# Kernel optimization log

Measured on AMD Instinct MI355X. Metric: run time of the kernel, lower is better.

## Reference

```python
import jax, jax.numpy as jnp
import numpy as np

# ---- graph / model config (matches init_kwargs) ----
N_FUNC, N_IN, N_OUT = 10000, 2000, 2000
C = 8          # hidden channels per function node (fix_hidden_channels=True)
K_FF = 16      # function->function in-degree
K_IF = 4       # out-edges per input node
LAYERS = 4     # shared ResBlock applied `layers` times
B = 64
EPS = 1e-5
N_NODES = N_FUNC + N_IN + N_OUT
H = N_FUNC * C


def _build_graph():
    """Homogeneous edge list ordered [f->f, in->f, f->out] like hetero2homo,
    plus COO indices of W1 (E x H) and W3 (H x E) per get_conv_indices."""
    rng = np.random.default_rng(0)
    ff_dst = np.repeat(np.arange(N_FUNC), K_FF)
    ff_src = rng.integers(0, N_FUNC, ff_dst.shape[0])
    if_src = np.repeat(np.arange(N_IN) + N_FUNC, K_IF)
    if_dst = rng.integers(0, N_FUNC, if_src.shape[0])
    fo_dst = np.arange(N_OUT) + N_FUNC + N_IN
    fo_src = rng.integers(0, N_FUNC, N_OUT)
    src = np.concatenate([ff_src, if_src, fo_src]).astype(np.int32)
    dst = np.concatenate([ff_dst, if_dst, fo_dst]).astype(np.int32)
    # W1: edge e (dst = function node j) -> hidden channels j*C + c
    e1 = np.nonzero(dst < N_FUNC)[0]
    w1_row = np.repeat(e1, C).astype(np.int32)
    w1_col = (np.repeat(dst[e1].astype(np.int64), C) * C + np.tile(np.arange(C), e1.shape[0])).astype(np.int32)
    # W3: hidden channel src*C + c -> edge e (src = function node)
    e3 = np.nonzero(src < N_FUNC)[0]
    w3_col = np.repeat(e3, C).astype(np.int32)
    w3_row = (np.repeat(src[e3].astype(np.int64), C) * C + np.tile(np.arange(C), e3.shape[0])).astype(np.int32)
    return src, dst, w1_row, w1_col, w3_row, w3_col


def setup_inputs() -> dict:
    src, dst, w1_row, w1_col, w3_row, w3_col = _build_graph()
    key = jax.random.key(0)
    k0, k1, k2 = jax.random.split(key, 3)
    s1 = 1.0 / np.sqrt(K_FF * C)   # fan-based scale for W1 values
    s3 = 1.0 / np.sqrt(C)          # fan-based scale for W3 values
    E = src.shape[0]
    return {
        "x": jax.random.normal(k0, (B, N_IN), jnp.float32),
        "w1_val": jax.random.normal(k1, (w1_row.shape[0],), jnp.float32) * s1,
        "b1": jnp.zeros((H,), jnp.float32),
        "w3_val": jax.random.normal(k2, (w3_row.shape[0],), jnp.float32) * s3,
        "b3": jnp.zeros((E,), jnp.float32),
        "gamma": jnp.ones((H,), jnp.float32),
        "beta": jnp.zeros((H,), jnp.float32),
        "edge_src": jnp.asarray(src),
        "edge_dst": jnp.asarray(dst),
        "w1_row": jnp.asarray(w1_row),
        "w1_col": jnp.asarray(w1_col),
        "w3_row": jnp.asarray(w3_row),
        "w3_col": jnp.asarray(w3_col),
    }


def _sparse_linear(xin, row, col, val, bias, out_dim):
    # out[b, j] = sum_{(i,j) in nz} W[i,j] * x[b,i] + bias[j]
    contrib = xin[:, row] * val                      # [B, nnz]
    out = jnp.zeros((xin.shape[0], out_dim), xin.dtype).at[:, col].add(contrib)
    return out + bias


def _group_layernorm(h, gamma, beta):
    # fix_hidden_channels=True => equal-size groups of C channels per function node
    g = h.reshape(h.shape[0], N_FUNC, C)
    mu = g.mean(-1, keepdims=True)
    var = g.var(-1, keepdims=True)
    g = (g - mu) * jax.lax.rsqrt(var + EPS)
    return g.reshape(h.shape[0], -1) * gamma + beta


def reference(x, w1_val, b1, w3_val, b3, gamma, beta,
              edge_src, edge_dst, w1_row, w1_col, w3_row, w3_col):
    E = edge_src.shape[0]
    # node values -> edge values (node2edge gathers source-node value per edge)
    x_node = jnp.zeros((x.shape[0], N_NODES), x.dtype).at[:, N_FUNC:N_FUNC + N_IN].set(x)
    xe = x_node[:, edge_src]                          # [B, E]

    def block(xe):  # ResBlock: lin1 -> GroupLayerNorm -> GELU -> lin3 -> +residual
        h = _sparse_linear(xe, w1_row, w1_col, w1_val, b1, H)
        h = _group_layernorm(h, gamma, beta)
        h = jax.nn.gelu(h, approximate=False)
        return _sparse_linear(h, w3_row, w3_col, w3_val, b3, E) + xe

    for _ in range(LAYERS):  # share_layers=True: same weights each layer
        xe = block(xe)
    xe = xe / LAYERS

    # edge2node: each output node has exactly one incoming edge (the last N_OUT edges)
    out_idx = edge_dst[-N_OUT:] - (N_FUNC + N_IN)
    out = jnp.zeros((xe.shape[0], N_OUT), xe.dtype).at[:, out_idx].set(xe[:, -N_OUT:])
    return out
```

## Files before the change

### kernel.cpp

```cpp
#include <hip/hip_runtime.h>

#define N_FUNC 10000
#define N_IN   2000
#define N_OUT  2000
#define CCH    8
#define K_FF   16
#define E_TOTAL 170000
#define E_FF    160000
#define E_W1    168000
#define E_IF    8000
#define BATCH   64
#define N_LAYERS 4
#define EPS_LN  1e-5f

#define SRC_CAP 64
#define IF_CAP  16

__device__ __forceinline__ float bf2f(unsigned short u) {
    unsigned int x = ((unsigned int)u) << 16;
    return __builtin_bit_cast(float, x);
}
__device__ __forceinline__ unsigned short f2bf(float f) {
    unsigned int x = __builtin_bit_cast(unsigned int, f);
    unsigned int r = x + 0x7FFFu + ((x >> 16) & 1u);
    return (unsigned short)(r >> 16);
}


__global__ void zero_cnt(int* __restrict__ a, int* __restrict__ b) {
    int i = blockIdx.x * blockDim.x + threadIdx.x;
    if (i < N_FUNC) { a[i] = 0; b[i] = 0; }
}

__global__ void fill_buckets(const int* __restrict__ src, const int* __restrict__ dst,
                             const float* __restrict__ x,
                             int* __restrict__ src_cnt, int* __restrict__ src_bkt,
                             int* __restrict__ if_cnt, int* __restrict__ if_bkt,
                             float* __restrict__ xT) {
    int i = blockIdx.x * blockDim.x + threadIdx.x;
    if (i < E_FF + N_OUT) {
        int e = (i < E_FF) ? i : (E_W1 + (i - E_FF));
        int s = src[e];
        int pos = atomicAdd(&src_cnt[s], 1);
        src_bkt[s * SRC_CAP + pos] = e;
    }
    if (i < E_IF) {
        int e = E_FF + i;
        int d = dst[e];
        int pos = atomicAdd(&if_cnt[d], 1);
        if_bkt[d * IF_CAP + pos] = e;
    }
    if (i < N_IN * BATCH) {
        int col = i >> 6, lane = i & 63;
        xT[col * BATCH + lane] = x[lane * N_IN + col];
    }
}


__device__ __forceinline__ void compute_h(
        const unsigned short* __restrict__ xe_old, const float* __restrict__ xT,
        const float* __restrict__ w1, const float* __restrict__ b1,
        const float* __restrict__ gamma, const float* __restrict__ beta,
        const float* __restrict__ b3, const int* __restrict__ if_cnt,
        const int* __restrict__ if_bkt, int f, int lane, int layer, bool first,
        float* __restrict__ hreg) {
    float acc[CCH];
    #pragma unroll
    for (int c = 0; c < CCH; c++) acc[c] = b1[f * CCH + c];

    if (!first) {
        float xv[K_FF];
        #pragma unroll
        for (int k = 0; k < K_FF; k++) xv[k] = bf2f(xe_old[(f * K_FF + k) * BATCH + lane]);
        #pragma unroll
        for (int k = 0; k < K_FF; k++) {
            int e = f * K_FF + k;
            #pragma unroll
            for (int c = 0; c < CCH; c++) acc[c] += xv[k] * w1[e * CCH + c];
        }
    }
    int icnt = if_cnt[f];
    float lf = (float)layer;
    for (int j = 0; j < icnt; j++) {
        int e = if_bkt[f * IF_CAP + j];
        int ii = (e - E_FF) >> 2;
        float xv = xT[ii * BATCH + lane] + lf * b3[e];
        #pragma unroll
        for (int c = 0; c < CCH; c++) acc[c] += xv * w1[e * CCH + c];
    }
    float mu = 0.f;
    #pragma unroll
    for (int c = 0; c < CCH; c++) mu += acc[c];
    mu *= 0.125f;
    float var = 0.f;
    #pragma unroll
    for (int c = 0; c < CCH; c++) { float d = acc[c] - mu; var += d * d; }
    var *= 0.125f;
    float rs = rsqrtf(var + EPS_LN);
    #pragma unroll
    for (int c = 0; c < CCH; c++) {
        float g = (acc[c] - mu) * rs * gamma[f * CCH + c] + beta[f * CCH + c];
        hreg[c] = 0.5f * g * (1.0f + erff(g * 0.70710678118654752f));
    }
}


template <bool FIRST>
__global__ __launch_bounds__(256) void layer_fused(
        const unsigned short* __restrict__ xe_old, unsigned short* __restrict__ xe_new,
        const float* __restrict__ xT, const float* __restrict__ w1,
        const float* __restrict__ b1, const float* __restrict__ gamma,
        const float* __restrict__ beta, const float* __restrict__ w3,
        const float* __restrict__ b3, const int* __restrict__ if_cnt,
        const int* __restrict__ if_bkt, const int* __restrict__ src_cnt,
        const int* __restrict__ src_bkt, int layer) {
    int wid = (blockIdx.x * blockDim.x + threadIdx.x) >> 6;
    int lane = threadIdx.x & 63;
    int f = __builtin_amdgcn_readfirstlane(wid);
    if (f >= N_FUNC) return;

    float hreg[CCH];
    compute_h(xe_old, xT, w1, b1, gamma, beta, b3, if_cnt, if_bkt,
              f, lane, layer, FIRST, hreg);

    const int* bkt = src_bkt + f * SRC_CAP;
    int ocnt = src_cnt[f];
    int j = 0;
    for (; j + 4 <= ocnt; j += 4) {
        int e0 = bkt[j], e1 = bkt[j + 1], e2 = bkt[j + 2], e3 = bkt[j + 3];
        float r0 = 0.f, r1 = 0.f, r2 = 0.f, r3 = 0.f;
        if (!FIRST) {
            r0 = bf2f(xe_old[e0 * BATCH + lane]);
            r1 = bf2f(xe_old[e1 * BATCH + lane]);
            r2 = bf2f(xe_old[e2 * BATCH + lane]);
            r3 = bf2f(xe_old[e3 * BATCH + lane]);
        }
        int p0 = (e0 < E_FF) ? e0 : (e0 - E_IF);
        int p1 = (e1 < E_FF) ? e1 : (e1 - E_IF);
        int p2 = (e2 < E_FF) ? e2 : (e2 - E_IF);
        int p3 = (e3 < E_FF) ? e3 : (e3 - E_IF);
        float a0 = b3[e0], a1 = b3[e1], a2 = b3[e2], a3 = b3[e3];
        #pragma unroll
        for (int c = 0; c < CCH; c++) {
            a0 += hreg[c] * w3[p0 * CCH + c];
            a1 += hreg[c] * w3[p1 * CCH + c];
            a2 += hreg[c] * w3[p2 * CCH + c];
            a3 += hreg[c] * w3[p3 * CCH + c];
        }
        xe_new[e0 * BATCH + lane] = f2bf(a0 + r0);
        xe_new[e1 * BATCH + lane] = f2bf(a1 + r1);
        xe_new[e2 * BATCH + lane] = f2bf(a2 + r2);
        xe_new[e3 * BATCH + lane] = f2bf(a3 + r3);
    }
    for (; j < ocnt; j++) {
        int e = bkt[j];
        int p = (e < E_FF) ? e : (e - E_IF);
        float a = b3[e];
        if (!FIRST) a += bf2f(xe_old[e * BATCH + lane]);
        #pragma unroll
        for (int c = 0; c < CCH; c++) a += hreg[c] * w3[p * CCH + c];
        xe_new[e * BATCH + lane] = f2bf(a);
    }
}


__global__ __launch_bounds__(256) void layer_last(
        const unsigned short* __restrict__ xe_old, const float* __restrict__ xT,
        const float* __restrict__ w1, const float* __restrict__ b1,
        const float* __restrict__ gamma, const float* __restrict__ beta,
        const float* __restrict__ w3, const float* __restrict__ b3,
        const int* __restrict__ if_cnt, const int* __restrict__ if_bkt,
        const int* __restrict__ edge_src, float* __restrict__ out) {
    int wid = (blockIdx.x * blockDim.x + threadIdx.x) >> 6;
    int lane = threadIdx.x & 63;
    int j = __builtin_amdgcn_readfirstlane(wid);
    if (j >= N_OUT) return;
    int e = E_W1 + j;
    int s = edge_src[e];

    float hreg[CCH];
    compute_h(xe_old, xT, w1, b1, gamma, beta, b3, if_cnt, if_bkt,
              s, lane, N_LAYERS - 1, false, hreg);

    int p = e - E_IF;
    float acc = bf2f(xe_old[e * BATCH + lane]) + b3[e];
    #pragma unroll
    for (int c = 0; c < CCH; c++) acc += hreg[c] * w3[p * CCH + c];
    out[lane * N_OUT + j] = acc * (1.0f / N_LAYERS);
}


extern "C" void kernel_launch(void* const* d_in, const int* in_sizes, int n_in,
                              void* d_out, int out_size, void* d_ws, size_t ws_size,
                              hipStream_t stream) {
    const float* x      = (const float*)d_in[0];
    const float* w1_val = (const float*)d_in[1];
    const float* b1     = (const float*)d_in[2];
    const float* w3_val = (const float*)d_in[3];
    const float* b3     = (const float*)d_in[4];
    const float* gamma  = (const float*)d_in[5];
    const float* beta   = (const float*)d_in[6];
    const int* edge_src = (const int*)d_in[7];
    const int* edge_dst = (const int*)d_in[8];
    float* out = (float*)d_out;

    char* base = (char*)d_ws;
    size_t off = 0;
    auto alloc = [&](size_t bytes) -> void* {
        void* p = base + off;
        off += (bytes + 255) & ~(size_t)255;
        return p;
    };
    unsigned short* xeA = (unsigned short*)alloc((size_t)E_TOTAL * BATCH * 2);
    unsigned short* xeB = (unsigned short*)alloc((size_t)E_TOTAL * BATCH * 2);
    float* xT     = (float*)alloc((size_t)N_IN * BATCH * 4);
    int* src_cnt  = (int*)alloc(N_FUNC * 4);
    int* if_cnt   = (int*)alloc(N_FUNC * 4);
    int* src_bkt  = (int*)alloc((size_t)N_FUNC * SRC_CAP * 4);
    int* if_bkt   = (int*)alloc((size_t)N_FUNC * IF_CAP * 4);
    (void)ws_size; (void)in_sizes; (void)n_in; (void)out_size;

    zero_cnt<<<(N_FUNC + 255) / 256, 256, 0, stream>>>(src_cnt, if_cnt);
    fill_buckets<<<(E_FF + N_OUT + 255) / 256, 256, 0, stream>>>(
        edge_src, edge_dst, x, src_cnt, src_bkt, if_cnt, if_bkt, xT);

    layer_fused<true><<<(N_FUNC * BATCH) / 256, 256, 0, stream>>>(
        xeA, xeB, xT, w1_val, b1, gamma, beta, w3_val, b3,
        if_cnt, if_bkt, src_cnt, src_bkt, 0);
    layer_fused<false><<<(N_FUNC * BATCH) / 256, 256, 0, stream>>>(
        xeB, xeA, xT, w1_val, b1, gamma, beta, w3_val, b3,
        if_cnt, if_bkt, src_cnt, src_bkt, 1);
    layer_fused<false><<<(N_FUNC * BATCH) / 256, 256, 0, stream>>>(
        xeA, xeB, xT, w1_val, b1, gamma, beta, w3_val, b3,
        if_cnt, if_bkt, src_cnt, src_bkt, 2);
    layer_last<<<(N_OUT * BATCH) / 256, 256, 0, stream>>>(
        xeB, xT, w1_val, b1, gamma, beta, w3_val, b3,
        if_cnt, if_bkt, edge_src, out);
}
```

Baseline: 194.0 us.

## Fuse all stages into one persistent cooperative kernel with grid syncs

Replaces the six separate launches (counter zeroing, bucket fill, three fused layers, final layer) with a single cooperative persistent kernel. Waves loop over function nodes with a grid stride, and grid.sync separates the stages. The scatter loop is also restructured into templated chunks of 8/4/2/1 so more loads are in flight. This removes launch gaps between kernels, but it caps the grid by occupancy, which reduces parallelism per stage, and it adds the cost of grid-wide barriers.

Result: slower. 668.7 us (+244.7%).

```diff
diff --git a/kernel.cpp b/kernel.cpp
--- a/kernel.cpp
+++ b/kernel.cpp
@@ -1,4 +1,7 @@
 #include <hip/hip_runtime.h>
+#include <hip/hip_cooperative_groups.h>
+
+namespace cg = cooperative_groups;
 
 #define N_FUNC 10000
 #define N_IN   2000
@@ -26,37 +29,6 @@
     return (unsigned short)(r >> 16);
 }
 
-
-__global__ void zero_cnt(int* __restrict__ a, int* __restrict__ b) {
-    int i = blockIdx.x * blockDim.x + threadIdx.x;
-    if (i < N_FUNC) { a[i] = 0; b[i] = 0; }
-}
-
-__global__ void fill_buckets(const int* __restrict__ src, const int* __restrict__ dst,
-                             const float* __restrict__ x,
-                             int* __restrict__ src_cnt, int* __restrict__ src_bkt,
-                             int* __restrict__ if_cnt, int* __restrict__ if_bkt,
-                             float* __restrict__ xT) {
-    int i = blockIdx.x * blockDim.x + threadIdx.x;
-    if (i < E_FF + N_OUT) {
-        int e = (i < E_FF) ? i : (E_W1 + (i - E_FF));
-        int s = src[e];
-        int pos = atomicAdd(&src_cnt[s], 1);
-        src_bkt[s * SRC_CAP + pos] = e;
-    }
-    if (i < E_IF) {
-        int e = E_FF + i;
-        int d = dst[e];
-        int pos = atomicAdd(&if_cnt[d], 1);
-        if_bkt[d * IF_CAP + pos] = e;
-    }
-    if (i < N_IN * BATCH) {
-        int col = i >> 6, lane = i & 63;
-        xT[col * BATCH + lane] = x[lane * N_IN + col];
-    }
-}
-
-
 __device__ __forceinline__ void compute_h(
         const unsigned short* __restrict__ xe_old, const float* __restrict__ xT,
         const float* __restrict__ w1, const float* __restrict__ b1,
@@ -74,9 +46,9 @@
         for (int k = 0; k < K_FF; k++) xv[k] = bf2f(xe_old[(f * K_FF + k) * BATCH + lane]);
         #pragma unroll
         for (int k = 0; k < K_FF; k++) {
-            int e = f * K_FF + k;
+            const float* wr = w1 + (size_t)(f * K_FF + k) * CCH;
             #pragma unroll
-            for (int c = 0; c < CCH; c++) acc[c] += xv[k] * w1[e * CCH + c];
+            for (int c = 0; c < CCH; c++) acc[c] += xv[k] * wr[c];
         }
     }
     int icnt = if_cnt[f];
@@ -85,8 +57,9 @@
         int e = if_bkt[f * IF_CAP + j];
         int ii = (e - E_FF) >> 2;
         float xv = xT[ii * BATCH + lane] + lf * b3[e];
-        #pragma unroll
-        for (int c = 0; c < CCH; c++) acc[c] += xv * w1[e * CCH + c];
+        const float* wr = w1 + (size_t)e * CCH;
+        #pragma unroll
+        for (int c = 0; c < CCH; c++) acc[c] += xv * wr[c];
     }
     float mu = 0.f;
     #pragma unroll
@@ -104,89 +77,107 @@
     }
 }
 
-
-template <bool FIRST>
-__global__ __launch_bounds__(256) void layer_fused(
+template <int CH>
+__device__ __forceinline__ void scat_chunk(
+        const int* __restrict__ bkt, int j, bool first,
         const unsigned short* __restrict__ xe_old, unsigned short* __restrict__ xe_new,
-        const float* __restrict__ xT, const float* __restrict__ w1,
-        const float* __restrict__ b1, const float* __restrict__ gamma,
-        const float* __restrict__ beta, const float* __restrict__ w3,
-        const float* __restrict__ b3, const int* __restrict__ if_cnt,
-        const int* __restrict__ if_bkt, const int* __restrict__ src_cnt,
-        const int* __restrict__ src_bkt, int layer) {
-    int wid = (blockIdx.x * blockDim.x + threadIdx.x) >> 6;
-    int lane = threadIdx.x & 63;
-    int f = __builtin_amdgcn_readfirstlane(wid);
-    if (f >= N_FUNC) return;
-
-    float hreg[CCH];
-    compute_h(xe_old, xT, w1, b1, gamma, beta, b3, if_cnt, if_bkt,
-              f, lane, layer, FIRST, hreg);
-
-    const int* bkt = src_bkt + f * SRC_CAP;
-    int ocnt = src_cnt[f];
-    int j = 0;
-    for (; j + 4 <= ocnt; j += 4) {
-        int e0 = bkt[j], e1 = bkt[j + 1], e2 = bkt[j + 2], e3 = bkt[j + 3];
-        float r0 = 0.f, r1 = 0.f, r2 = 0.f, r3 = 0.f;
-        if (!FIRST) {
-            r0 = bf2f(xe_old[e0 * BATCH + lane]);
-            r1 = bf2f(xe_old[e1 * BATCH + lane]);
-            r2 = bf2f(xe_old[e2 * BATCH + lane]);
-            r3 = bf2f(xe_old[e3 * BATCH + lane]);
+        const float* __restrict__ w3, const float* __restrict__ b3,
+        const float* __restrict__ hreg, int lane) {
+    int e[CH];
+    float r[CH];
+    #pragma unroll
+    for (int q = 0; q < CH; q++) e[q] = bkt[j + q];
+    #pragma unroll
+    for (int q = 0; q < CH; q++)
+        r[q] = first ? 0.f : bf2f(xe_old[(size_t)e[q] * BATCH + lane]);
+    #pragma unroll
+    for (int q = 0; q < CH; q++) {
+        int p = (e[q] < E_FF) ? e[q] : (e[q] - E_IF);
+        const float* wr = w3 + (size_t)p * CCH;
+        float a = b3[e[q]] + r[q];
+        #pragma unroll
+        for (int c = 0; c < CCH; c++) a += hreg[c] * wr[c];
+        xe_new[(size_t)e[q] * BATCH + lane] = f2bf(a);
+    }
+}
+
+
+__global__ __launch_bounds__(256, 4) void gsnn_all(
+        const float* __restrict__ x, const float* __restrict__ w1,
+        const float* __restrict__ b1, const float* __restrict__ w3,
+        const float* __restrict__ b3, const float* __restrict__ gamma,
+        const float* __restrict__ beta, const int* __restrict__ esrc,
+        const int* __restrict__ edst, float* __restrict__ out,
+        unsigned short* __restrict__ xeA, unsigned short* __restrict__ xeB,
+        float* __restrict__ xT, int* __restrict__ src_cnt, int* __restrict__ if_cnt,
+        int* __restrict__ src_bkt, int* __restrict__ if_bkt) {
+    cg::grid_group grid = cg::this_grid();
+    const int tid = blockIdx.x * blockDim.x + threadIdx.x;
+    const int nthr = gridDim.x * blockDim.x;
+    const int lane = threadIdx.x & 63;
+    const int wave0 = tid >> 6;
+    const int nwaves = nthr >> 6;
+
+    for (int i = tid; i < N_FUNC; i += nthr) { src_cnt[i] = 0; if_cnt[i] = 0; }
+    grid.sync();
+
+    for (int i = tid; i < E_FF + N_OUT; i += nthr) {
+        int e = (i < E_FF) ? i : (E_W1 + (i - E_FF));
+        int s = esrc[e];
+        int pos = atomicAdd(&src_cnt[s], 1);
+        src_bkt[s * SRC_CAP + pos] = e;
+    }
+    for (int i = tid; i < E_IF; i += nthr) {
+        int e = E_FF + i;
+        int d = edst[e];
+        int pos = atomicAdd(&if_cnt[d], 1);
+        if_bkt[d * IF_CAP + pos] = e;
+    }
+    for (int i = tid; i < N_IN * BATCH; i += nthr) {
+        int col = i >> 6, b = i & 63;
+        xT[col * BATCH + b] = x[b * N_IN + col];
+    }
+    grid.sync();
+
+    const unsigned short* oldp = xeA;
+    unsigned short* newp = xeB;
+    for (int l = 0; l < 3; l++) {
+        const bool first = (l == 0);
+        for (int f0 = wave0; f0 < N_FUNC; f0 += nwaves) {
+            int f = __builtin_amdgcn_readfirstlane(f0);
+            float hreg[CCH];
+            compute_h(oldp, xT, w1, b1, gamma, beta, b3, if_cnt, if_bkt,
+                      f, lane, l, first, hreg);
+            const int* bkt = src_bkt + f * SRC_CAP;
+            int ocnt = src_cnt[f];
+            int j = 0;
+            for (; j + 8 <= ocnt; j += 8)
+                scat_chunk<8>(bkt, j, first, oldp, newp, w3, b3, hreg, lane);
+            for (; j + 4 <= ocnt; j += 4)
+                scat_chunk<4>(bkt, j, first, oldp, newp, w3, b3, hreg, lane);
+            for (; j + 2 <= ocnt; j += 2)
+                scat_chunk<2>(bkt, j, first, oldp, newp, w3, b3, hreg, lane);
+            for (; j < ocnt; j++)
+                scat_chunk<1>(bkt, j, first, oldp, newp, w3, b3, hreg, lane);
         }
-        int p0 = (e0 < E_FF) ? e0 : (e0 - E_IF);
-        int p1 = (e1 < E_FF) ? e1 : (e1 - E_IF);
-        int p2 = (e2 < E_FF) ? e2 : (e2 - E_IF);
-        int p3 = (e3 < E_FF) ? e3 : (e3 - E_IF);
-        float a0 = b3[e0], a1 = b3[e1], a2 = b3[e2], a3 = b3[e3];
-        #pragma unroll
-        for (int c = 0; c < CCH; c++) {
-            a0 += hreg[c] * w3[p0 * CCH + c];
-            a1 += hreg[c] * w3[p1 * CCH + c];
-            a2 += hreg[c] * w3[p2 * CCH + c];
-            a3 += hreg[c] * w3[p3 * CCH + c];
-        }
-        xe_new[e0 * BATCH + lane] = f2bf(a0 + r0);
-        xe_new[e1 * BATCH + lane] = f2bf(a1 + r1);
-        xe_new[e2 * BATCH + lane] = f2bf(a2 + r2);
-        xe_new[e3 * BATCH + lane] = f2bf(a3 + r3);
-    }
-    for (; j < ocnt; j++) {
-        int e = bkt[j];
-        int p = (e < E_FF) ? e : (e - E_IF);
-        float a = b3[e];
-        if (!FIRST) a += bf2f(xe_old[e * BATCH + lane]);
-        #pragma unroll
-        for (int c = 0; c < CCH; c++) a += hreg[c] * w3[p * CCH + c];
-        xe_new[e * BATCH + lane] = f2bf(a);
-    }
-}
-
-
-__global__ __launch_bounds__(256) void layer_last(
-        const unsigned short* __restrict__ xe_old, const float* __restrict__ xT,
-        const float* __restrict__ w1, const float* __restrict__ b1,
-        const float* __restrict__ gamma, const float* __restrict__ beta,
-        const float* __restrict__ w3, const float* __restrict__ b3,
-        const int* __restrict__ if_cnt, const int* __restrict__ if_bkt,
-        const int* __restrict__ edge_src, float* __restrict__ out) {
-    int wid = (blockIdx.x * blockDim.x + threadIdx.x) >> 6;
-    int lane = threadIdx.x & 63;
-    int j = __builtin_amdgcn_readfirstlane(wid);
-    if (j >= N_OUT) return;
-    int e = E_W1 + j;
-    int s = edge_src[e];
-
-    float hreg[CCH];
-    compute_h(xe_old, xT, w1, b1, gamma, beta, b3, if_cnt, if_bkt,
-              s, lane, N_LAYERS - 1, false, hreg);
-
-    int p = e - E_IF;
-    float acc = bf2f(xe_old[e * BATCH + lane]) + b3[e];
-    #pragma unroll
-    for (int c = 0; c < CCH; c++) acc += hreg[c] * w3[p * CCH + c];
-    out[lane * N_OUT + j] = acc * (1.0f / N_LAYERS);
+        grid.sync();
+        const unsigned short* t = oldp; oldp = newp; newp = (unsigned short*)t;
+    }
+
+    for (int j0 = wave0; j0 < N_OUT; j0 += nwaves) {
+        int j = __builtin_amdgcn_readfirstlane(j0);
+        int e = E_W1 + j;
+        int s = __builtin_amdgcn_readfirstlane(esrc[e]);
+        float hreg[CCH];
+        compute_h(oldp, xT, w1, b1, gamma, beta, b3, if_cnt, if_bkt,
+                  s, lane, N_LAYERS - 1, false, hreg);
+        int p = e - E_IF;
+        const float* wr = w3 + (size_t)p * CCH;
+        float acc = bf2f(oldp[(size_t)e * BATCH + lane]) + b3[e];
+        #pragma unroll
+        for (int c = 0; c < CCH; c++) acc += hreg[c] * wr[c];
+        out[lane * N_OUT + j] = acc * (1.0f / N_LAYERS);
+    }
 }
 
 
@@ -220,20 +211,17 @@
     int* if_bkt   = (int*)alloc((size_t)N_FUNC * IF_CAP * 4);
     (void)ws_size; (void)in_sizes; (void)n_in; (void)out_size;
 
-    zero_cnt<<<(N_FUNC + 255) / 256, 256, 0, stream>>>(src_cnt, if_cnt);
-    fill_buckets<<<(E_FF + N_OUT + 255) / 256, 256, 0, stream>>>(
-        edge_src, edge_dst, x, src_cnt, src_bkt, if_cnt, if_bkt, xT);
-
-    layer_fused<true><<<(N_FUNC * BATCH) / 256, 256, 0, stream>>>(
-        xeA, xeB, xT, w1_val, b1, gamma, beta, w3_val, b3,
-        if_cnt, if_bkt, src_cnt, src_bkt, 0);
-    layer_fused<false><<<(N_FUNC * BATCH) / 256, 256, 0, stream>>>(
-        xeB, xeA, xT, w1_val, b1, gamma, beta, w3_val, b3,
-        if_cnt, if_bkt, src_cnt, src_bkt, 1);
-    layer_fused<false><<<(N_FUNC * BATCH) / 256, 256, 0, stream>>>(
-        xeA, xeB, xT, w1_val, b1, gamma, beta, w3_val, b3,
-        if_cnt, if_bkt, src_cnt, src_bkt, 2);
-    layer_last<<<(N_OUT * BATCH) / 256, 256, 0, stream>>>(
-        xeB, xT, w1_val, b1, gamma, beta, w3_val, b3,
-        if_cnt, if_bkt, edge_src, out);
-}
+    int nb = 0;
+    hipOccupancyMaxActiveBlocksPerMultiprocessor(&nb, gsnn_all, 256, 0);
+    if (nb < 1) nb = 1;
+    int grid = nb * 256;
+    if (grid > 2048) grid = 2048;
+
+    void* args[] = {
+        (void*)&x, (void*)&w1_val, (void*)&b1, (void*)&w3_val, (void*)&b3,
+        (void*)&gamma, (void*)&beta, (void*)&edge_src, (void*)&edge_dst,
+        (void*)&out, (void*)&xeA, (void*)&xeB, (void*)&xT,
+        (void*)&src_cnt, (void*)&if_cnt, (void*)&src_bkt, (void*)&if_bkt
+    };
+    hipLaunchCooperativeKernel(gsnn_all, dim3(grid), dim3(256), args, 0, stream);
+}
```
